# Optimization experiments

Hardware: AMD Instinct MI355X
Metric: run time of the kernel (lower is better)

## Reference

```python
import jax, jax.numpy as jnp
import numpy as np


def setup_inputs() -> dict:
    key = jax.random.key(0)
    k1, k2, k3, k4, k5 = jax.random.split(key, 5)
    B, S, D = 16, 1024, 64
    query = jax.random.normal(k1, (B, S, D), dtype=jnp.float32)
    key_t = jax.random.normal(k2, (B, S, D), dtype=jnp.float32)
    value = jax.random.normal(k3, (B, S, D), dtype=jnp.float32)
    t_m = jax.random.uniform(k4, (B, S, S), dtype=jnp.float32)
    g_m = jax.random.uniform(k5, (B, S, S), dtype=jnp.float32)
    # causal mask [S, S]: 1 where attention allowed
    mask = jnp.tril(jnp.ones((S, S), dtype=jnp.int32))
    return {"query": query, "key": key_t, "value": value,
            "t_m": t_m, "g_m": g_m, "mask": mask}


def _bias(m):
    # per-batch max over all S*S entries, then abs difference
    mx = jnp.max(m.reshape(m.shape[0], -1), axis=1)  # [B]
    return jnp.abs(m - mx[:, None, None])            # [B, S, S]


def reference(query, key, value, t_m, g_m, mask):
    d_k = query.shape[-1]
    # NOTE: source divides by d_k, not sqrt(d_k)
    scores = jnp.einsum('bqd,bkd->bqk', query, key) / d_k  # [B, S, S]
    scores = scores + _bias(t_m) + _bias(g_m)
    scores = jnp.where(mask[None, :, :] == 0, jnp.float32(-1e9), scores)
    p_attn = jax.nn.softmax(scores, axis=-1)
    return jnp.einsum('bqk,bkd->bqd', p_attn, value)
```

## Files before the change

### kernel.cpp

```cpp
#include <hip/hip_runtime.h>
#include <hip/hip_bf16.h>

#define B_  16
#define S_  1024
#define D_  64

typedef __attribute__((ext_vector_type(8))) short bf16x8;
typedef __attribute__((ext_vector_type(4))) float f32x4;

__device__ __forceinline__ unsigned short f2bf_u(float f) {
    __hip_bfloat16 h = __float2bfloat16(f);
    return __builtin_bit_cast(unsigned short, h);
}
__device__ __forceinline__ short f2bf(float f) {
    return (short)f2bf_u(f);
}
__device__ __forceinline__ unsigned pk2(float a, float b) {
    return (unsigned)f2bf_u(a) | ((unsigned)f2bf_u(b) << 16);
}

__global__ __launch_bounds__(256) void prep_kernel(
    const float* __restrict__ K, const float* __restrict__ V,
    unsigned short* __restrict__ Kbf, unsigned short* __restrict__ VT)
{
    const int bid = blockIdx.x;
    if (bid < 512) {
        const size_t i = ((size_t)bid * 256 + threadIdx.x) * 8;
        const float4 x = *(const float4*)(K + i);
        const float4 y = *(const float4*)(K + i + 4);
        uint4 o = { pk2(x.x, x.y), pk2(x.z, x.w), pk2(y.x, y.y), pk2(y.z, y.w) };
        *(uint4*)(Kbf + i) = o;
    } else {
        const int i  = (bid - 512) * 256 + threadIdx.x;
        const int d  = i & 63;
        const int kg = (i >> 6) & 127;
        const int b  = i >> 13;
        const float* vp = V + ((size_t)b * S_ + (size_t)kg * 8) * D_ + d;
        const float v0 = vp[0],   v1 = vp[64],  v2 = vp[128], v3 = vp[192];
        const float v4 = vp[256], v5 = vp[320], v6 = vp[384], v7 = vp[448];
        uint4 o = { pk2(v0, v1), pk2(v2, v3), pk2(v4, v5), pk2(v6, v7) };
        *(uint4*)(VT + ((size_t)b * D_ + d) * S_ + kg * 8) = o;
    }
}

__global__ __launch_bounds__(256, 4) void attn_mfma_pre(
    const unsigned short* __restrict__ Kbf, const unsigned short* __restrict__ VT,
    const float* __restrict__ Q, const float* __restrict__ t_m,
    const float* __restrict__ g_m, float* __restrict__ out)
{
    __shared__ __align__(16) char smem[17920];
    unsigned short (*s_p)[136] = (unsigned short (*)[136])smem;
    float (*s_bias)[16][40] = (float (*)[16][40])(smem + 4608);
    float* cmb = (float*)smem;
    float* cml = (float*)(smem + 17408);

    const int bid = blockIdx.x;
    const int b   = bid & 15;
    const int g   = bid >> 4;
    const int qt  = (g < 32) ? (63 - g) : (g - 32);
    const int qb  = qt << 4;
    const int tid = threadIdx.x;
    const int w   = tid >> 6;
    const int ln  = tid & 63;
    const int lg  = ln >> 4;
    const int lm  = ln & 15;

    const size_t biasb = (size_t)b * S_ * S_;
    const int brow = ln >> 3;
    const int bc4  = ln & 7;
    const float* tmb0 = t_m + biasb + (size_t)(qb + brow) * S_ + 4 * bc4;
    const float* gmb0 = g_m + biasb + (size_t)(qb + brow) * S_ + 4 * bc4;
    const float* tmb1 = tmb0 + 8 * S_;
    const float* gmb1 = gmb0 + 8 * S_;

    const unsigned short* Kbb = Kbf + ((size_t)(b * S_) + lm) * D_ + 8 * lg;
    const unsigned short* vt0 = VT + ((size_t)(b * D_) + 0  + lm) * S_ + 8 * lg;
    const unsigned short* vt1 = VT + ((size_t)(b * D_) + 16 + lm) * S_ + 8 * lg;
    const unsigned short* vt2 = VT + ((size_t)(b * D_) + 32 + lm) * S_ + 8 * lg;
    const unsigned short* vt3 = VT + ((size_t)(b * D_) + 48 + lm) * S_ + 8 * lg;

    bf16x8 qa[2];
    #pragma unroll
    for (int ks = 0; ks < 2; ++ks) {
        const float* qp = Q + ((size_t)(b * S_) + qb + lm) * D_ + 32 * ks + 8 * lg;
        const float4 x = *(const float4*)qp;
        const float4 y = *(const float4*)(qp + 4);
        bf16x8 f;
        f[0] = f2bf(x.x * 0.015625f); f[1] = f2bf(x.y * 0.015625f);
        f[2] = f2bf(x.z * 0.015625f); f[3] = f2bf(x.w * 0.015625f);
        f[4] = f2bf(y.x * 0.015625f); f[5] = f2bf(y.y * 0.015625f);
        f[6] = f2bf(y.z * 0.015625f); f[7] = f2bf(y.w * 0.015625f);
        qa[ks] = f;
    }

    float lpart[4] = {0.f, 0.f, 0.f, 0.f};
    const f32x4 z4 = {0.f, 0.f, 0.f, 0.f};
    f32x4 oacc[4] = {z4, z4, z4, z4};

    const int ntw = ((qb + 15 - 32 * w) >> 7) + 1;

    for (int t = 0; t < ntw; ++t) {
        const int ke = (t << 7) + 32 * w;

        const float4 bt0 = *(const float4*)(tmb0 + ke);
        const float4 bg0 = *(const float4*)(gmb0 + ke);
        const float4 bt1 = *(const float4*)(tmb1 + ke);
        const float4 bg1 = *(const float4*)(gmb1 + ke);

        const unsigned short* kp = Kbb + (size_t)ke * D_;
        const bf16x8 kf00 = *(const bf16x8*)kp;
        const bf16x8 kf01 = *(const bf16x8*)(kp + 32);
        const bf16x8 kf10 = *(const bf16x8*)(kp + 16 * D_);
        const bf16x8 kf11 = *(const bf16x8*)(kp + 16 * D_ + 32);

        const bf16x8 vb0 = *(const bf16x8*)(vt0 + ke);
        const bf16x8 vb1 = *(const bf16x8*)(vt1 + ke);
        const bf16x8 vb2 = *(const bf16x8*)(vt2 + ke);
        const bf16x8 vb3 = *(const bf16x8*)(vt3 + ke);

        {
            float4 u0, u1;
            u0.x = bt0.x + bg0.x;  u0.y = bt0.y + bg0.y;
            u0.z = bt0.z + bg0.z;  u0.w = bt0.w + bg0.w;
            u1.x = bt1.x + bg1.x;  u1.y = bt1.y + bg1.y;
            u1.z = bt1.z + bg1.z;  u1.w = bt1.w + bg1.w;
            *(float4*)&s_bias[w][brow][4 * bc4]     = u0;
            *(float4*)&s_bias[w][8 + brow][4 * bc4] = u1;
        }

        f32x4 sa[2] = {z4, z4};
        sa[0] = __builtin_amdgcn_mfma_f32_16x16x32_bf16(qa[0], kf00, sa[0], 0, 0, 0);
        sa[0] = __builtin_amdgcn_mfma_f32_16x16x32_bf16(qa[1], kf01, sa[0], 0, 0, 0);
        sa[1] = __builtin_amdgcn_mfma_f32_16x16x32_bf16(qa[0], kf10, sa[1], 0, 0, 0);
        sa[1] = __builtin_amdgcn_mfma_f32_16x16x32_bf16(qa[1], kf11, sa[1], 0, 0, 0);

        float bsum[2][4];
        #pragma unroll
        for (int nf = 0; nf < 2; ++nf)
            #pragma unroll
            for (int r = 0; r < 4; ++r)
                bsum[nf][r] = s_bias[w][4 * lg + r][16 * nf + lm];

        float p[2][4];
        #pragma unroll
        for (int r = 0; r < 4; ++r) {
            const int qg = qb + 4 * lg + r;
            const float p0 = (ke + lm > qg)
                           ? 0.f : __expf(sa[0][r] - bsum[0][r]);
            const float p1 = (ke + 16 + lm > qg)
                           ? 0.f : __expf(sa[1][r] - bsum[1][r]);
            p[0][r] = p0;  p[1][r] = p1;
            lpart[r] += p0 + p1;
        }

        #pragma unroll
        for (int nf = 0; nf < 2; ++nf)
            #pragma unroll
            for (int r = 0; r < 4; ++r)
                s_p[4 * lg + r][32 * w + 16 * nf + lm] = f2bf_u(p[nf][r]);
        asm volatile("s_waitcnt lgkmcnt(0)" ::: "memory");
        const bf16x8 pa = *(const bf16x8*)&s_p[lm][32 * w + 8 * lg];

        oacc[0] = __builtin_amdgcn_mfma_f32_16x16x32_bf16(pa, vb0, oacc[0], 0, 0, 0);
        oacc[1] = __builtin_amdgcn_mfma_f32_16x16x32_bf16(pa, vb1, oacc[1], 0, 0, 0);
        oacc[2] = __builtin_amdgcn_mfma_f32_16x16x32_bf16(pa, vb2, oacc[2], 0, 0, 0);
        oacc[3] = __builtin_amdgcn_mfma_f32_16x16x32_bf16(pa, vb3, oacc[3], 0, 0, 0);
    }

    #pragma unroll
    for (int off = 1; off < 16; off <<= 1)
        #pragma unroll
        for (int r = 0; r < 4; ++r)
            lpart[r] += __shfl_xor(lpart[r], off, 64);

    __syncthreads();
    #pragma unroll
    for (int nd = 0; nd < 4; ++nd)
        #pragma unroll
        for (int r = 0; r < 4; ++r)
            cmb[(w * 16 + 4 * lg + r) * 68 + 16 * nd + lm] = oacc[nd][r];
    if (lm == 0) {
        #pragma unroll
        for (int r = 0; r < 4; ++r)
            cml[w * 16 + 4 * lg + r] = lpart[r];
    }
    __syncthreads();
    {
        const int q = tid >> 4, c = tid & 15;
        const float lt = cml[q] + cml[16 + q] + cml[32 + q] + cml[48 + q];
        const float inv = 1.f / lt;
        float4 acc = make_float4(0.f, 0.f, 0.f, 0.f);
        #pragma unroll
        for (int i = 0; i < 4; ++i) {
            const float4 v = *(const float4*)&cmb[(i * 16 + q) * 68 + 4 * c];
            acc.x += v.x;  acc.y += v.y;
            acc.z += v.z;  acc.w += v.w;
        }
        acc.x *= inv; acc.y *= inv; acc.z *= inv; acc.w *= inv;
        *(float4*)(out + ((size_t)(b * S_) + qb + q) * D_ + 4 * c) = acc;
    }
}

__global__ __launch_bounds__(256, 4) void attn_mfma_kernel(
    const float* __restrict__ Q, const float* __restrict__ K,
    const float* __restrict__ V, const float* __restrict__ t_m,
    const float* __restrict__ g_m, float* __restrict__ out)
{
    __shared__ __align__(16) char smem[17920];
    unsigned short (*s_p)[136] = (unsigned short (*)[136])smem;
    float* cmb = (float*)smem;
    float* cml = (float*)(smem + 17408);

    const int bid = blockIdx.x;
    const int b   = bid & 15;
    const int g   = bid >> 4;
    const int qt  = (g < 32) ? (63 - g) : (g - 32);
    const int qb  = qt << 4;
    const int tid = threadIdx.x;
    const int w   = tid >> 6;
    const int ln  = tid & 63;
    const int lg  = ln >> 4;
    const int lm  = ln & 15;

    const size_t kvb   = (size_t)(b * S_) * D_;
    const size_t biasb = (size_t)b * S_ * S_;
    const float* Kb = K + kvb;
    const float* Vb = V + kvb;

    bf16x8 qa[2];
    #pragma unroll
    for (int ks = 0; ks < 2; ++ks) {
        const float* qp = Q + ((size_t)(b * S_) + qb + lm) * D_ + 32 * ks + 8 * lg;
        const float4 x = *(const float4*)qp;
        const float4 y = *(const float4*)(qp + 4);
        bf16x8 f;
        f[0] = f2bf(x.x); f[1] = f2bf(x.y);
        f[2] = f2bf(x.z); f[3] = f2bf(x.w);
        f[4] = f2bf(y.x); f[5] = f2bf(y.y);
        f[6] = f2bf(y.z); f[7] = f2bf(y.w);
        qa[ks] = f;
    }

    float mrun[4] = {-1e30f, -1e30f, -1e30f, -1e30f};
    float lrun[4] = {0.f, 0.f, 0.f, 0.f};
    const f32x4 z4 = {0.f, 0.f, 0.f, 0.f};
    f32x4 oacc[4] = {z4, z4, z4, z4};

    const int ntw = ((qb + 15 - 32 * w) >> 7) + 1;

    for (int t = 0; t < ntw; ++t) {
        const int ke = (t << 7) + 32 * w;

        bf16x8 kf[2][2];
        #pragma unroll
        for (int nf = 0; nf < 2; ++nf)
            #pragma unroll
            for (int ks = 0; ks < 2; ++ks) {
                const float* kp = Kb + (size_t)(ke + 16 * nf + lm) * D_ + 32 * ks + 8 * lg;
                const float4 x = *(const float4*)kp;
                const float4 y = *(const float4*)(kp + 4);
                bf16x8 f;
                f[0] = f2bf(x.x); f[1] = f2bf(x.y);
                f[2] = f2bf(x.z); f[3] = f2bf(x.w);
                f[4] = f2bf(y.x); f[5] = f2bf(y.y);
                f[6] = f2bf(y.z); f[7] = f2bf(y.w);
                kf[nf][ks] = f;
            }

        float bt[2][4], bg[2][4];
        #pragma unroll
        for (int nf = 0; nf < 2; ++nf)
            #pragma unroll
            for (int r = 0; r < 4; ++r) {
                const size_t off = biasb + (size_t)(qb + 4 * lg + r) * S_
                                 + ke + 16 * nf + lm;
                bt[nf][r] = t_m[off];
                bg[nf][r] = g_m[off];
            }

        f32x4 sa[2] = {z4, z4};
        #pragma unroll
        for (int nf = 0; nf < 2; ++nf)
            #pragma unroll
            for (int ks = 0; ks < 2; ++ks)
                sa[nf] = __builtin_amdgcn_mfma_f32_16x16x32_bf16(
                    qa[ks], kf[nf][ks], sa[nf], 0, 0, 0);

        float vf[4][8];
        #pragma unroll
        for (int nd = 0; nd < 4; ++nd)
            #pragma unroll
            for (int j = 0; j < 8; ++j)
                vf[nd][j] = Vb[(size_t)(ke + 8 * lg + j) * D_ + 16 * nd + lm];

        float p[2][4], tmax[4];
        #pragma unroll
        for (int r = 0; r < 4; ++r) {
            const int qg = qb + 4 * lg + r;
            float s0 = sa[0][r] * (1.f / 64.f) - bt[0][r] - bg[0][r];
            float s1 = sa[1][r] * (1.f / 64.f) - bt[1][r] - bg[1][r];
            if (ke + lm > qg)      s0 = -1e30f;
            if (ke + 16 + lm > qg) s1 = -1e30f;
            p[0][r] = s0;  p[1][r] = s1;
            tmax[r] = fmaxf(s0, s1);
        }
        #pragma unroll
        for (int off = 1; off < 16; off <<= 1)
            #pragma unroll
            for (int r = 0; r < 4; ++r)
                tmax[r] = fmaxf(tmax[r], __shfl_xor(tmax[r], off, 64));

        #pragma unroll
        for (int r = 0; r < 4; ++r) {
            const float mn = fmaxf(mrun[r], tmax[r]);
            const float a  = __expf(mrun[r] - mn);
            mrun[r] = mn;
            const float p0 = __expf(p[0][r] - mn);
            const float p1 = __expf(p[1][r] - mn);
            p[0][r] = p0;  p[1][r] = p1;
            float rs = p0 + p1;
            #pragma unroll
            for (int off = 1; off < 16; off <<= 1)
                rs += __shfl_xor(rs, off, 64);
            lrun[r] = lrun[r] * a + rs;
            #pragma unroll
            for (int nd = 0; nd < 4; ++nd) oacc[nd][r] *= a;
        }

        #pragma unroll
        for (int nf = 0; nf < 2; ++nf)
            #pragma unroll
            for (int r = 0; r < 4; ++r)
                s_p[4 * lg + r][32 * w + 16 * nf + lm] = f2bf_u(p[nf][r]);
        asm volatile("s_waitcnt lgkmcnt(0)" ::: "memory");
        const bf16x8 pa = *(const bf16x8*)&s_p[lm][32 * w + 8 * lg];

        #pragma unroll
        for (int nd = 0; nd < 4; ++nd) {
            bf16x8 vb;
            #pragma unroll
            for (int j = 0; j < 8; ++j) vb[j] = f2bf(vf[nd][j]);
            oacc[nd] = __builtin_amdgcn_mfma_f32_16x16x32_bf16(
                pa, vb, oacc[nd], 0, 0, 0);
        }
    }

    __syncthreads();
    #pragma unroll
    for (int nd = 0; nd < 4; ++nd)
        #pragma unroll
        for (int r = 0; r < 4; ++r)
            cmb[(w * 16 + 4 * lg + r) * 68 + 16 * nd + lm] = oacc[nd][r];
    if (lm == 0) {
        #pragma unroll
        for (int r = 0; r < 4; ++r) {
            cml[w * 32 + 4 * lg + r]      = mrun[r];
            cml[w * 32 + 16 + 4 * lg + r] = lrun[r];
        }
    }
    __syncthreads();
    {
        const int q = tid >> 4, c = tid & 15;
        float mm[4], sc[4];
        float ms = -1e30f;
        #pragma unroll
        for (int i = 0; i < 4; ++i) { mm[i] = cml[i * 32 + q]; ms = fmaxf(ms, mm[i]); }
        float lt = 0.f;
        #pragma unroll
        for (int i = 0; i < 4; ++i) {
            sc[i] = __expf(mm[i] - ms);
            lt += cml[i * 32 + 16 + q] * sc[i];
        }
        const float inv = 1.f / lt;
        float4 acc = make_float4(0.f, 0.f, 0.f, 0.f);
        #pragma unroll
        for (int i = 0; i < 4; ++i) {
            const float4 v = *(const float4*)&cmb[(i * 16 + q) * 68 + 4 * c];
            acc.x += v.x * sc[i];  acc.y += v.y * sc[i];
            acc.z += v.z * sc[i];  acc.w += v.w * sc[i];
        }
        acc.x *= inv; acc.y *= inv; acc.z *= inv; acc.w *= inv;
        *(float4*)(out + ((size_t)(b * S_) + qb + q) * D_ + 4 * c) = acc;
    }
}

extern "C" void kernel_launch(void* const* d_in, const int* in_sizes, int n_in,
                              void* d_out, int out_size, void* d_ws, size_t ws_size,
                              hipStream_t stream) {
    const float* Q   = (const float*)d_in[0];
    const float* Kp  = (const float*)d_in[1];
    const float* V   = (const float*)d_in[2];
    const float* t_m = (const float*)d_in[3];
    const float* g_m = (const float*)d_in[4];

    const size_t n_kv = (size_t)B_ * S_ * D_;
    const size_t need = 2 * n_kv * sizeof(unsigned short);
    if (ws_size >= need) {
        unsigned short* Kbf = (unsigned short*)d_ws;
        unsigned short* VT  = Kbf + n_kv;
        prep_kernel<<<1024, 256, 0, stream>>>(Kp, V, Kbf, VT);
        attn_mfma_pre<<<1024, 256, 0, stream>>>(Kbf, VT, Q, t_m, g_m,
                                                (float*)d_out);
    } else {
        attn_mfma_kernel<<<1024, 256, 0, stream>>>(Q, Kp, V, t_m, g_m,
                                                   (float*)d_out);
    }
}
```

Measured before the change: 31.72 us.

## Process two 32-key sub-tiles per wave iteration with interleaved loads and MFMAs

Each wave now covers 64 keys per loop iteration (stride 256 across the block) instead of 32. The second half's K/V fragment loads are issued while the first half's QK MFMAs and softmax run, and the bias loads for both halves are issued together. The goal is more memory requests in flight and better overlap of global loads with MFMA and exp work. In exchange it uses more shared memory and registers, and the coarser causal granularity computes more masked work near the diagonal.

```diff
diff --git a/kernel.cpp b/kernel.cpp
--- a/kernel.cpp
+++ b/kernel.cpp
@@ -48,9 +48,9 @@
     const float* __restrict__ Q, const float* __restrict__ t_m,
     const float* __restrict__ g_m, float* __restrict__ out)
 {
-    __shared__ __align__(16) char smem[17920];
-    unsigned short (*s_p)[136] = (unsigned short (*)[136])smem;
-    float (*s_bias)[16][40] = (float (*)[16][40])(smem + 4608);
+    __shared__ __align__(16) char smem[26880];
+    unsigned short (*s_p)[264] = (unsigned short (*)[264])smem;
+    float (*s_bias)[16][72] = (float (*)[16][72])(smem + 8448);
     float* cmb = (float*)smem;
     float* cml = (float*)(smem + 17408);
 
@@ -97,74 +97,121 @@
     const f32x4 z4 = {0.f, 0.f, 0.f, 0.f};
     f32x4 oacc[4] = {z4, z4, z4, z4};
 
-    const int ntw = ((qb + 15 - 32 * w) >> 7) + 1;
+    const int base_w = 64 * w;
+    const int ntw = ((qb + 15 - base_w) >> 8) + 1;
 
     for (int t = 0; t < ntw; ++t) {
-        const int ke = (t << 7) + 32 * w;
-
-        const float4 bt0 = *(const float4*)(tmb0 + ke);
-        const float4 bg0 = *(const float4*)(gmb0 + ke);
-        const float4 bt1 = *(const float4*)(tmb1 + ke);
-        const float4 bg1 = *(const float4*)(gmb1 + ke);
-
-        const unsigned short* kp = Kbb + (size_t)ke * D_;
-        const bf16x8 kf00 = *(const bf16x8*)kp;
-        const bf16x8 kf01 = *(const bf16x8*)(kp + 32);
-        const bf16x8 kf10 = *(const bf16x8*)(kp + 16 * D_);
-        const bf16x8 kf11 = *(const bf16x8*)(kp + 16 * D_ + 32);
-
-        const bf16x8 vb0 = *(const bf16x8*)(vt0 + ke);
-        const bf16x8 vb1 = *(const bf16x8*)(vt1 + ke);
-        const bf16x8 vb2 = *(const bf16x8*)(vt2 + ke);
-        const bf16x8 vb3 = *(const bf16x8*)(vt3 + ke);
+        const int ke = (t << 8) + base_w;
+
+        const float4 bt0a = *(const float4*)(tmb0 + ke);
+        const float4 bg0a = *(const float4*)(gmb0 + ke);
+        const float4 bt1a = *(const float4*)(tmb1 + ke);
+        const float4 bg1a = *(const float4*)(gmb1 + ke);
+        const float4 bt0b = *(const float4*)(tmb0 + ke + 32);
+        const float4 bg0b = *(const float4*)(gmb0 + ke + 32);
+        const float4 bt1b = *(const float4*)(tmb1 + ke + 32);
+        const float4 bg1b = *(const float4*)(gmb1 + ke + 32);
+
+        const unsigned short* kpA = Kbb + (size_t)ke * D_;
+        const bf16x8 kfA00 = *(const bf16x8*)kpA;
+        const bf16x8 kfA01 = *(const bf16x8*)(kpA + 32);
+        const bf16x8 kfA10 = *(const bf16x8*)(kpA + 16 * D_);
+        const bf16x8 kfA11 = *(const bf16x8*)(kpA + 16 * D_ + 32);
 
         {
-            float4 u0, u1;
-            u0.x = bt0.x + bg0.x;  u0.y = bt0.y + bg0.y;
-            u0.z = bt0.z + bg0.z;  u0.w = bt0.w + bg0.w;
-            u1.x = bt1.x + bg1.x;  u1.y = bt1.y + bg1.y;
-            u1.z = bt1.z + bg1.z;  u1.w = bt1.w + bg1.w;
-            *(float4*)&s_bias[w][brow][4 * bc4]     = u0;
-            *(float4*)&s_bias[w][8 + brow][4 * bc4] = u1;
-        }
-
-        f32x4 sa[2] = {z4, z4};
-        sa[0] = __builtin_amdgcn_mfma_f32_16x16x32_bf16(qa[0], kf00, sa[0], 0, 0, 0);
-        sa[0] = __builtin_amdgcn_mfma_f32_16x16x32_bf16(qa[1], kf01, sa[0], 0, 0, 0);
-        sa[1] = __builtin_amdgcn_mfma_f32_16x16x32_bf16(qa[0], kf10, sa[1], 0, 0, 0);
-        sa[1] = __builtin_amdgcn_mfma_f32_16x16x32_bf16(qa[1], kf11, sa[1], 0, 0, 0);
-
-        float bsum[2][4];
-        #pragma unroll
-        for (int nf = 0; nf < 2; ++nf)
-            #pragma unroll
-            for (int r = 0; r < 4; ++r)
-                bsum[nf][r] = s_bias[w][4 * lg + r][16 * nf + lm];
-
-        float p[2][4];
-        #pragma unroll
-        for (int r = 0; r < 4; ++r) {
-            const int qg = qb + 4 * lg + r;
-            const float p0 = (ke + lm > qg)
-                           ? 0.f : __expf(sa[0][r] - bsum[0][r]);
-            const float p1 = (ke + 16 + lm > qg)
-                           ? 0.f : __expf(sa[1][r] - bsum[1][r]);
-            p[0][r] = p0;  p[1][r] = p1;
-            lpart[r] += p0 + p1;
-        }
-
-        #pragma unroll
-        for (int nf = 0; nf < 2; ++nf)
-            #pragma unroll
-            for (int r = 0; r < 4; ++r)
-                s_p[4 * lg + r][32 * w + 16 * nf + lm] = f2bf_u(p[nf][r]);
+            float4 u0, u1, u2, u3;
+            u0.x = bt0a.x + bg0a.x;  u0.y = bt0a.y + bg0a.y;
+            u0.z = bt0a.z + bg0a.z;  u0.w = bt0a.w + bg0a.w;
+            u1.x = bt1a.x + bg1a.x;  u1.y = bt1a.y + bg1a.y;
+            u1.z = bt1a.z + bg1a.z;  u1.w = bt1a.w + bg1a.w;
+            u2.x = bt0b.x + bg0b.x;  u2.y = bt0b.y + bg0b.y;
+            u2.z = bt0b.z + bg0b.z;  u2.w = bt0b.w + bg0b.w;
+            u3.x = bt1b.x + bg1b.x;  u3.y = bt1b.y + bg1b.y;
+            u3.z = bt1b.z + bg1b.z;  u3.w = bt1b.w + bg1b.w;
+            *(float4*)&s_bias[w][brow][4 * bc4]          = u0;
+            *(float4*)&s_bias[w][8 + brow][4 * bc4]      = u1;
+            *(float4*)&s_bias[w][brow][32 + 4 * bc4]     = u2;
+            *(float4*)&s_bias[w][8 + brow][32 + 4 * bc4] = u3;
+        }
+
+        f32x4 saA0 = z4, saA1 = z4;
+        saA0 = __builtin_amdgcn_mfma_f32_16x16x32_bf16(qa[0], kfA00, saA0, 0, 0, 0);
+        saA0 = __builtin_amdgcn_mfma_f32_16x16x32_bf16(qa[1], kfA01, saA0, 0, 0, 0);
+        saA1 = __builtin_amdgcn_mfma_f32_16x16x32_bf16(qa[0], kfA10, saA1, 0, 0, 0);
+        saA1 = __builtin_amdgcn_mfma_f32_16x16x32_bf16(qa[1], kfA11, saA1, 0, 0, 0);
+
+        const unsigned short* kpB = Kbb + (size_t)(ke + 32) * D_;
+        const bf16x8 kfB00 = *(const bf16x8*)kpB;
+        const bf16x8 kfB01 = *(const bf16x8*)(kpB + 32);
+        const bf16x8 kfB10 = *(const bf16x8*)(kpB + 16 * D_);
+        const bf16x8 kfB11 = *(const bf16x8*)(kpB + 16 * D_ + 32);
+        const bf16x8 vbA0 = *(const bf16x8*)(vt0 + ke);
+        const bf16x8 vbA1 = *(const bf16x8*)(vt1 + ke);
+        const bf16x8 vbA2 = *(const bf16x8*)(vt2 + ke);
+        const bf16x8 vbA3 = *(const bf16x8*)(vt3 + ke);
+
+        {
+            float p[2][4];
+            #pragma unroll
+            for (int r = 0; r < 4; ++r) {
+                const int qg = qb + 4 * lg + r;
+                const float b0 = s_bias[w][4 * lg + r][lm];
+                const float b1 = s_bias[w][4 * lg + r][16 + lm];
+                const float p0 = (ke + lm > qg)      ? 0.f : __expf(saA0[r] - b0);
+                const float p1 = (ke + 16 + lm > qg) ? 0.f : __expf(saA1[r] - b1);
+                p[0][r] = p0;  p[1][r] = p1;
+                lpart[r] += p0 + p1;
+            }
+            #pragma unroll
+            for (int nf = 0; nf < 2; ++nf)
+                #pragma unroll
+                for (int r = 0; r < 4; ++r)
+                    s_p[4 * lg + r][64 * w + 16 * nf + lm] = f2bf_u(p[nf][r]);
+        }
         asm volatile("s_waitcnt lgkmcnt(0)" ::: "memory");
-        const bf16x8 pa = *(const bf16x8*)&s_p[lm][32 * w + 8 * lg];
-
-        oacc[0] = __builtin_amdgcn_mfma_f32_16x16x32_bf16(pa, vb0, oacc[0], 0, 0, 0);
-        oacc[1] = __builtin_amdgcn_mfma_f32_16x16x32_bf16(pa, vb1, oacc[1], 0, 0, 0);
-        oacc[2] = __builtin_amdgcn_mfma_f32_16x16x32_bf16(pa, vb2, oacc[2], 0, 0, 0);
-        oacc[3] = __builtin_amdgcn_mfma_f32_16x16x32_bf16(pa, vb3, oacc[3], 0, 0, 0);
+        const bf16x8 paA = *(const bf16x8*)&s_p[lm][64 * w + 8 * lg];
+
+        const bf16x8 vbB0 = *(const bf16x8*)(vt0 + ke + 32);
+        const bf16x8 vbB1 = *(const bf16x8*)(vt1 + ke + 32);
+        const bf16x8 vbB2 = *(const bf16x8*)(vt2 + ke + 32);
+        const bf16x8 vbB3 = *(const bf16x8*)(vt3 + ke + 32);
+
+        oacc[0] = __builtin_amdgcn_mfma_f32_16x16x32_bf16(paA, vbA0, oacc[0], 0, 0, 0);
+        oacc[1] = __builtin_amdgcn_mfma_f32_16x16x32_bf16(paA, vbA1, oacc[1], 0, 0, 0);
+        oacc[2] = __builtin_amdgcn_mfma_f32_16x16x32_bf16(paA, vbA2, oacc[2], 0, 0, 0);
+        oacc[3] = __builtin_amdgcn_mfma_f32_16x16x32_bf16(paA, vbA3, oacc[3], 0, 0, 0);
+
+        f32x4 saB0 = z4, saB1 = z4;
+        saB0 = __builtin_amdgcn_mfma_f32_16x16x32_bf16(qa[0], kfB00, saB0, 0, 0, 0);
+        saB0 = __builtin_amdgcn_mfma_f32_16x16x32_bf16(qa[1], kfB01, saB0, 0, 0, 0);
+        saB1 = __builtin_amdgcn_mfma_f32_16x16x32_bf16(qa[0], kfB10, saB1, 0, 0, 0);
+        saB1 = __builtin_amdgcn_mfma_f32_16x16x32_bf16(qa[1], kfB11, saB1, 0, 0, 0);
+
+        {
+            float p[2][4];
+            #pragma unroll
+            for (int r = 0; r < 4; ++r) {
+                const int qg = qb + 4 * lg + r;
+                const float b0 = s_bias[w][4 * lg + r][32 + lm];
+                const float b1 = s_bias[w][4 * lg + r][48 + lm];
+                const float p0 = (ke + 32 + lm > qg) ? 0.f : __expf(saB0[r] - b0);
+                const float p1 = (ke + 48 + lm > qg) ? 0.f : __expf(saB1[r] - b1);
+                p[0][r] = p0;  p[1][r] = p1;
+                lpart[r] += p0 + p1;
+            }
+            #pragma unroll
+            for (int nf = 0; nf < 2; ++nf)
+                #pragma unroll
+                for (int r = 0; r < 4; ++r)
+                    s_p[4 * lg + r][64 * w + 32 + 16 * nf + lm] = f2bf_u(p[nf][r]);
+        }
+        asm volatile("s_waitcnt lgkmcnt(0)" ::: "memory");
+        const bf16x8 paB = *(const bf16x8*)&s_p[lm][64 * w + 32 + 8 * lg];
+
+        oacc[0] = __builtin_amdgcn_mfma_f32_16x16x32_bf16(paB, vbB0, oacc[0], 0, 0, 0);
+        oacc[1] = __builtin_amdgcn_mfma_f32_16x16x32_bf16(paB, vbB1, oacc[1], 0, 0, 0);
+        oacc[2] = __builtin_amdgcn_mfma_f32_16x16x32_bf16(paB, vbB2, oacc[2], 0, 0, 0);
+        oacc[3] = __builtin_amdgcn_mfma_f32_16x16x32_bf16(paB, vbB3, oacc[3], 0, 0, 0);
     }
 
     #pragma unroll
```

New measurement: 33.04 us. +4.2%, slower.
